# Kernel tuning notes

Measured on AMD Instinct MI355X. Metric: run time of the kernel, lower is better.

The kernel has to match this reference:

```python
import jax, jax.numpy as jnp
import numpy as np

B, S, IN, OUT = 4, 2048, 4096, 4096


def setup_inputs() -> dict:
    key = jax.random.key(0)
    kx, kw, kb = jax.random.split(key, 3)
    x = jax.random.randint(kx, (B, S, IN), -127, 128, dtype=jnp.int8)
    weight = jax.random.randint(kw, (OUT, IN), -127, 128, dtype=jnp.int8)
    # original module initializes bias to zeros(int32); use random int32 to exercise the add
    bias = jax.random.randint(kb, (1, OUT), -1000, 1000, dtype=jnp.int32)
    return {"x": x, "weight": weight, "bias": bias}


def reference(x, weight, bias):
    x_shape = x.shape
    x2 = x.reshape(-1, x_shape[-1])  # [tokens, IN], int8
    # dot_general with preferred_element_type=int32 -> int8 inputs, int32 accumulate
    y = jax.lax.dot_general(
        x2, weight,
        dimension_numbers=(((1,), (1,)), ((), ())),
        preferred_element_type=jnp.int32,
    )  # [tokens, OUT] int32
    y = y + bias  # broadcast [1, OUT] int32
    return y.reshape(*x_shape[:-1], -1)
```

## Files before the change

### kernel.cpp

```cpp
#include <hip/hip_runtime.h>
#include <stdint.h>

#define M_TOT 8192
#define N_TOT 4096
#define K_TOT 4096

typedef int v4i  __attribute__((ext_vector_type(4)));
typedef int v16i __attribute__((ext_vector_type(16)));

__device__ __forceinline__ void gload_lds16(const void* g, void* l) {
    __builtin_amdgcn_global_load_lds(
        (const __attribute__((address_space(1))) unsigned int*)g,
        (__attribute__((address_space(3))) unsigned int*)l,
        16, 0, 0);
}

__global__ __launch_bounds__(256) void pack_i32_to_i8(
        const int* __restrict__ src, signed char* __restrict__ dst, int n16) {
    const int idx = blockIdx.x * 256 + threadIdx.x;
    if (idx >= n16) return;
    const int4* s = (const int4*)src;
    int4 a = s[idx * 4 + 0];
    int4 b = s[idx * 4 + 1];
    int4 c = s[idx * 4 + 2];
    int4 d = s[idx * 4 + 3];
    int4 p;
    p.x = (a.x & 255) | ((a.y & 255) << 8) | ((a.z & 255) << 16) | (a.w << 24);
    p.y = (b.x & 255) | ((b.y & 255) << 8) | ((b.z & 255) << 16) | (b.w << 24);
    p.z = (c.x & 255) | ((c.y & 255) << 8) | ((c.z & 255) << 16) | (c.w << 24);
    p.w = (d.x & 255) | ((d.y & 255) << 8) | ((d.z & 255) << 16) | (d.w << 24);
    ((int4*)dst)[idx] = p;
}

__global__ __launch_bounds__(256) void i8gemm_bias(
        const signed char* __restrict__ x,
        const signed char* __restrict__ w,
        const int* __restrict__ bias,
        int* __restrict__ out) {
    __shared__ __align__(16) signed char la[128 * 64];
    __shared__ __align__(16) signed char lb[128 * 64];

    const int tid  = threadIdx.x;
    const int lane = tid & 63;
    const int wave = tid >> 6;
    const int wm   = (wave >> 1) * 64;
    const int wn   = (wave & 1) * 64;
    const int bm0  = blockIdx.y * 128;
    const int bn0  = blockIdx.x * 128;

    const int l31 = lane & 31;
    const int kh  = lane >> 5;

    const int bv0 = bias[bn0 + wn + l31];
    const int bv1 = bias[bn0 + wn + 32 + l31];
    v16i acc[2][2];
#pragma unroll
    for (int i = 0; i < 2; ++i)
#pragma unroll
        for (int r = 0; r < 16; ++r) {
            acc[i][0][r] = bv0;
            acc[i][1][r] = bv1;
        }

    const signed char* ga = x + (long)bm0 * K_TOT;
    const signed char* gb = w + (long)bn0 * K_TOT;

    int srow[2];
    int scol[2];
    signed char* lwa[2];
    signed char* lwb[2];
#pragma unroll
    for (int i = 0; i < 2; ++i) {
        const int g = i * 256 + tid;
        srow[i] = g >> 2;
        scol[i] = ((g & 3) ^ ((srow[i] >> 1) & 3)) * 16;
        lwa[i] = la + i * 4096 + wave * 1024;
        lwb[i] = lb + i * 4096 + wave * 1024;
    }

    const int arow[2] = { wm + l31, wm + 32 + l31 };
    const int brow[2] = { wn + l31, wn + 32 + l31 };

    for (int kt = 0; kt < K_TOT / 64; ++kt) {
        const int k0 = kt * 64;
        __syncthreads();
#pragma unroll
        for (int i = 0; i < 2; ++i) {
            gload_lds16(ga + (long)srow[i] * K_TOT + k0 + scol[i], lwa[i]);
            gload_lds16(gb + (long)srow[i] * K_TOT + k0 + scol[i], lwb[i]);
        }
        __syncthreads();

        v4i af[2][2], bf[2][2];
#pragma unroll
        for (int i = 0; i < 2; ++i) {
            const int raA = arow[i];
            const int swA = (raA >> 1) & 3;
            const int raB = brow[i];
            const int swB = (raB >> 1) & 3;
#pragma unroll
            for (int kk = 0; kk < 2; ++kk) {
                const int cA = ((kk * 2 + kh) ^ swA) * 16;
                const int cB = ((kk * 2 + kh) ^ swB) * 16;
                af[i][kk] = *(const v4i*)(la + raA * 64 + cA);
                bf[i][kk] = *(const v4i*)(lb + raB * 64 + cB);
            }
        }

#pragma unroll
        for (int kk = 0; kk < 2; ++kk)
#pragma unroll
            for (int i = 0; i < 2; ++i)
#pragma unroll
                for (int j = 0; j < 2; ++j)
                    acc[i][j] = __builtin_amdgcn_mfma_i32_32x32x32_i8(
                        af[i][kk], bf[j][kk], acc[i][j], 0, 0, 0);
    }

#pragma unroll
    for (int i = 0; i < 2; ++i) {
        const int mbase = bm0 + wm + i * 32 + 4 * kh;
#pragma unroll
        for (int j = 0; j < 2; ++j) {
            const int n = bn0 + wn + j * 32 + l31;
#pragma unroll
            for (int r = 0; r < 16; ++r) {
                const int m = mbase + (r & 3) + 8 * (r >> 2);
                out[(long)m * N_TOT + n] = acc[i][j][r];
            }
        }
    }
}

extern "C" void kernel_launch(void* const* d_in, const int* in_sizes, int n_in,
                              void* d_out, int out_size, void* d_ws, size_t ws_size,
                              hipStream_t stream) {
    const int* x32  = (const int*)d_in[0];
    const int* w32  = (const int*)d_in[1];
    const int* bias = (const int*)d_in[2];
    int*       out  = (int*)d_out;

    signed char* xp = (signed char*)d_ws;
    signed char* wp = (signed char*)d_ws + (size_t)M_TOT * K_TOT;

    const int n16x = (M_TOT * K_TOT) / 16;
    const int n16w = (N_TOT * K_TOT) / 16;
    pack_i32_to_i8<<<n16x / 256, 256, 0, stream>>>(x32, xp, n16x);
    pack_i32_to_i8<<<n16w / 256, 256, 0, stream>>>(w32, wp, n16w);

    dim3 grid(N_TOT / 128, M_TOT / 128);
    i8gemm_bias<<<grid, 256, 0, stream>>>(xp, wp, bias, out);
}
```

Measured before the change: 438.1 us.

## Use single-wave 128x128 GEMM blocks and finer-grained int8 packing

The GEMM block drops from four waves to one wave that computes the whole 128x128 tile with a 4x4 grid of 32x32 MFMA accumulators, which raises register-level operand reuse. One wave now issues all the global-to-LDS loads itself, and occupancy falls to one wave per block under launch_bounds(64,1). The pack kernel now has each thread read one int4 and write one int instead of sixteen values per thread. The single wave must hide load latency alone, with no double buffering and heavy accumulator register pressure.

```diff
diff --git a/kernel.cpp b/kernel.cpp
--- a/kernel.cpp
+++ b/kernel.cpp
@@ -16,23 +16,14 @@
 }
 
 __global__ __launch_bounds__(256) void pack_i32_to_i8(
-        const int* __restrict__ src, signed char* __restrict__ dst, int n16) {
+        const int4* __restrict__ src, int* __restrict__ dst, int n4) {
     const int idx = blockIdx.x * 256 + threadIdx.x;
-    if (idx >= n16) return;
-    const int4* s = (const int4*)src;
-    int4 a = s[idx * 4 + 0];
-    int4 b = s[idx * 4 + 1];
-    int4 c = s[idx * 4 + 2];
-    int4 d = s[idx * 4 + 3];
-    int4 p;
-    p.x = (a.x & 255) | ((a.y & 255) << 8) | ((a.z & 255) << 16) | (a.w << 24);
-    p.y = (b.x & 255) | ((b.y & 255) << 8) | ((b.z & 255) << 16) | (b.w << 24);
-    p.z = (c.x & 255) | ((c.y & 255) << 8) | ((c.z & 255) << 16) | (c.w << 24);
-    p.w = (d.x & 255) | ((d.y & 255) << 8) | ((d.z & 255) << 16) | (d.w << 24);
-    ((int4*)dst)[idx] = p;
+    if (idx >= n4) return;
+    const int4 a = src[idx];
+    dst[idx] = (a.x & 255) | ((a.y & 255) << 8) | ((a.z & 255) << 16) | (a.w << 24);
 }
 
-__global__ __launch_bounds__(256) void i8gemm_bias(
+__global__ __launch_bounds__(64, 1) void i8gemm_bias(
         const signed char* __restrict__ x,
         const signed char* __restrict__ w,
         const int* __restrict__ bias,
@@ -40,89 +31,63 @@
     __shared__ __align__(16) signed char la[128 * 64];
     __shared__ __align__(16) signed char lb[128 * 64];
 
-    const int tid  = threadIdx.x;
-    const int lane = tid & 63;
-    const int wave = tid >> 6;
-    const int wm   = (wave >> 1) * 64;
-    const int wn   = (wave & 1) * 64;
+    const int lane = threadIdx.x;
+    const int l31  = lane & 31;
+    const int kh   = lane >> 5;
     const int bm0  = blockIdx.y * 128;
     const int bn0  = blockIdx.x * 128;
 
-    const int l31 = lane & 31;
-    const int kh  = lane >> 5;
+    int bv[4];
+#pragma unroll
+    for (int j = 0; j < 4; ++j) bv[j] = bias[bn0 + j * 32 + l31];
+    v16i acc[4][4];
+#pragma unroll
+    for (int i = 0; i < 4; ++i)
+#pragma unroll
+        for (int j = 0; j < 4; ++j)
+#pragma unroll
+            for (int r = 0; r < 16; ++r) acc[i][j][r] = bv[j];
 
-    const int bv0 = bias[bn0 + wn + l31];
-    const int bv1 = bias[bn0 + wn + 32 + l31];
-    v16i acc[2][2];
-#pragma unroll
-    for (int i = 0; i < 2; ++i)
-#pragma unroll
-        for (int r = 0; r < 16; ++r) {
-            acc[i][0][r] = bv0;
-            acc[i][1][r] = bv1;
-        }
+    const int fc = (lane & 3) ^ ((lane >> 3) & 3);
+    const signed char* pa = x + (long)(bm0 + (lane >> 2)) * K_TOT + fc * 16;
+    const signed char* pb = w + (long)(bn0 + (lane >> 2)) * K_TOT + fc * 16;
 
-    const signed char* ga = x + (long)bm0 * K_TOT;
-    const signed char* gb = w + (long)bn0 * K_TOT;
-
-    int srow[2];
-    int scol[2];
-    signed char* lwa[2];
-    signed char* lwb[2];
-#pragma unroll
-    for (int i = 0; i < 2; ++i) {
-        const int g = i * 256 + tid;
-        srow[i] = g >> 2;
-        scol[i] = ((g & 3) ^ ((srow[i] >> 1) & 3)) * 16;
-        lwa[i] = la + i * 4096 + wave * 1024;
-        lwb[i] = lb + i * 4096 + wave * 1024;
-    }
-
-    const int arow[2] = { wm + l31, wm + 32 + l31 };
-    const int brow[2] = { wn + l31, wn + 32 + l31 };
+    const int swr = (l31 >> 1) & 3;
 
     for (int kt = 0; kt < K_TOT / 64; ++kt) {
-        const int k0 = kt * 64;
+        const long k0 = (long)kt * 64;
         __syncthreads();
 #pragma unroll
-        for (int i = 0; i < 2; ++i) {
-            gload_lds16(ga + (long)srow[i] * K_TOT + k0 + scol[i], lwa[i]);
-            gload_lds16(gb + (long)srow[i] * K_TOT + k0 + scol[i], lwb[i]);
+        for (int i = 0; i < 8; ++i) {
+            gload_lds16(pa + k0 + (long)i * 16 * K_TOT, la + i * 1024);
+            gload_lds16(pb + k0 + (long)i * 16 * K_TOT, lb + i * 1024);
         }
         __syncthreads();
 
-        v4i af[2][2], bf[2][2];
 #pragma unroll
-        for (int i = 0; i < 2; ++i) {
-            const int raA = arow[i];
-            const int swA = (raA >> 1) & 3;
-            const int raB = brow[i];
-            const int swB = (raB >> 1) & 3;
+        for (int kk = 0; kk < 2; ++kk) {
+            const int cs = ((kk * 2 + kh) ^ swr) * 16;
+            v4i af[4], bf[4];
 #pragma unroll
-            for (int kk = 0; kk < 2; ++kk) {
-                const int cA = ((kk * 2 + kh) ^ swA) * 16;
-                const int cB = ((kk * 2 + kh) ^ swB) * 16;
-                af[i][kk] = *(const v4i*)(la + raA * 64 + cA);
-                bf[i][kk] = *(const v4i*)(lb + raB * 64 + cB);
+            for (int i = 0; i < 4; ++i) {
+                af[i] = *(const v4i*)(la + (i * 32 + l31) * 64 + cs);
+                bf[i] = *(const v4i*)(lb + (i * 32 + l31) * 64 + cs);
             }
+#pragma unroll
+            for (int i = 0; i < 4; ++i)
+#pragma unroll
+                for (int j = 0; j < 4; ++j)
+                    acc[i][j] = __builtin_amdgcn_mfma_i32_32x32x32_i8(
+                        af[i], bf[j], acc[i][j], 0, 0, 0);
         }
-
-#pragma unroll
-        for (int kk = 0; kk < 2; ++kk)
-#pragma unroll
-            for (int i = 0; i < 2; ++i)
-#pragma unroll
-                for (int j = 0; j < 2; ++j)
-                    acc[i][j] = __builtin_amdgcn_mfma_i32_32x32x32_i8(
-                        af[i][kk], bf[j][kk], acc[i][j], 0, 0, 0);
     }
 
 #pragma unroll
-    for (int i = 0; i < 2; ++i) {
-        const int mbase = bm0 + wm + i * 32 + 4 * kh;
+    for (int i = 0; i < 4; ++i) {
+        const int mbase = bm0 + i * 32 + 4 * kh;
 #pragma unroll
-        for (int j = 0; j < 2; ++j) {
-            const int n = bn0 + wn + j * 32 + l31;
+        for (int j = 0; j < 4; ++j) {
+            const int n = bn0 + j * 32 + l31;
 #pragma unroll
             for (int r = 0; r < 16; ++r) {
                 const int m = mbase + (r & 3) + 8 * (r >> 2);
@@ -143,11 +108,11 @@
     signed char* xp = (signed char*)d_ws;
     signed char* wp = (signed char*)d_ws + (size_t)M_TOT * K_TOT;
 
-    const int n16x = (M_TOT * K_TOT) / 16;
-    const int n16w = (N_TOT * K_TOT) / 16;
-    pack_i32_to_i8<<<n16x / 256, 256, 0, stream>>>(x32, xp, n16x);
-    pack_i32_to_i8<<<n16w / 256, 256, 0, stream>>>(w32, wp, n16w);
+    const int n4x = (M_TOT * K_TOT) / 4;
+    const int n4w = (N_TOT * K_TOT) / 4;
+    pack_i32_to_i8<<<n4x / 256, 256, 0, stream>>>((const int4*)x32, (int*)xp, n4x);
+    pack_i32_to_i8<<<n4w / 256, 256, 0, stream>>>((const int4*)w32, (int*)wp, n4w);
 
     dim3 grid(N_TOT / 128, M_TOT / 128);
-    i8gemm_bias<<<grid, 256, 0, stream>>>(xp, wp, bias, out);
+    i8gemm_bias<<<grid, 64, 0, stream>>>(xp, wp, bias, out);
 }
```

New measurement: 415.2 us. 5.2% less time.
